# Kernel optimization log

Measured on AMD Instinct MI355X. Metric: run time of the kernel, lower is better.

## Reference

```python
import jax, jax.numpy as jnp
import numpy as np

CHANNEL = 16
KERNEL_SIZE = 5

def _gaussian3d_weight(channel, kernel_size):
    sigma = kernel_size / 6.0
    r = jnp.arange(-(kernel_size // 2), (kernel_size + 1) // 2, dtype=jnp.float32) ** 2
    # sum of squared offsets along each axis -> isotropic Gaussian
    k3 = r[None, None, :] + r[None, :, None] + r[:, None, None]
    k3 = jnp.exp(-k3 / (2.0 * sigma ** 2))
    k3 = k3 / k3.sum()
    # depthwise weight: [C_out=C, C_in/groups=1, kD, kH, kW]
    return jnp.broadcast_to(k3, (channel, 1, kernel_size, kernel_size, kernel_size))

def setup_inputs() -> dict:
    key = jax.random.key(0)
    x = jax.random.normal(key, (2, CHANNEL, 64, 128, 128), dtype=jnp.float32)
    weight = _gaussian3d_weight(CHANNEL, KERNEL_SIZE)
    return {"x": x, "weight": weight}

def reference(x, weight):
    # depthwise Conv3d, padding='same', groups=channel, no bias
    return jax.lax.conv_general_dilated(
        x, weight,
        window_strides=(1, 1, 1),
        padding='SAME',
        dimension_numbers=('NCDHW', 'OIDHW', 'NCDHW'),
        feature_group_count=CHANNEL,
    )
```

## Files before the change

kernel.cpp:

```cpp
#include <hip/hip_runtime.h>


#define DD 64
#define HH 128
#define WW 128
#define NC 16
#define ZCHUNK 16
#define SLICE (HH * WW)

typedef const __attribute__((address_space(1))) unsigned int g_u32;
typedef __attribute__((address_space(3))) unsigned int l_u32;

__global__ __launch_bounds__(256, 6)
void gauss3d_kernel(const float* __restrict__ x,
                    const float* __restrict__ wt,
                    float* __restrict__ out)
{
    __shared__ float raw[4][2][6][WW];
    __shared__ float wlds[16];

    const int tid  = threadIdx.x;
    const int w    = tid >> 6;
    const int lane = tid & 63;
    const int by   = blockIdx.x * 8;
    const int slab = blockIdx.y;
    const int z0   = blockIdx.z * ZCHUNK;
    const int ch   = slab & (NC - 1);

    const float* xs = x   + (size_t)slab * DD * SLICE;
    float*       os = out + (size_t)slab * DD * SLICE;

    if (tid < 15) {
        const int a = tid / 5, q = tid % 5;
        const float* wp = wt + ch * 125;
        float s = 0.f;
        for (int u = 0; u < 5; ++u)
            for (int v = 0; v < 5; ++v) {
                const int i0 = (a == 0) ? q : u;
                const int j0 = (a == 1) ? q : ((a == 0) ? u : v);
                const int k0 = (a == 2) ? q : v;
                s += wp[i0 * 25 + j0 * 5 + k0];
            }
        wlds[a * 5 + q] = s;
    }
    __syncthreads();

    const int sub    = lane >> 5;
    const int lane31 = lane & 31;
    const int col    = lane31 << 2;
    const int wy0    = by + w * 2;
    const int gy     = wy0 + sub;

    int so[3];
#pragma unroll
    for (int k = 0; k < 3; ++k) {
        const int gr = min(max(wy0 - 2 + 2 * k + sub, 0), HH - 1);
        so[k] = gr * WW + col;
    }

    float wzc[5], wxc[5], wyv[5];
#pragma unroll
    for (int i = 0; i < 5; ++i) {
        wzc[i] = wlds[i];
        wxc[i] = wlds[10 + i];
        const int r = gy - 2 + i;
        wyv[i] = (r >= 0 && r < HH) ? wlds[5 + i] : 0.f;
    }

    const int zbase = z0 - 2;

#define STAGE(ZS, B)                                                         \
    {                                                                        \
        const int zc = min(max((ZS), 0), DD - 1);                            \
        const float* sl = xs + (size_t)zc * SLICE;                           \
        _Pragma("unroll")                                                    \
        for (int k = 0; k < 3; ++k)                                          \
            __builtin_amdgcn_global_load_lds((g_u32*)(sl + so[k]),           \
                (l_u32*)(&raw[w][(B)][2 * k][0]), 16, 0, 0);                 \
    }

    float4 r0, r1, r2, r3, r4;
    r0 = r1 = r2 = r3 = r4 = make_float4(0.f, 0.f, 0.f, 0.f);

    STAGE(zbase, 0)

#define GSTEP(o0, o1, o2, o3, o4, I, WAIT)                                   \
    {                                                                        \
        const int zs = zbase + (I);                                          \
        STAGE(zs + 1, ((I) + 1) & 1)                                         \
        asm volatile("s_waitcnt vmcnt(" #WAIT ")" ::: "memory");             \
        __builtin_amdgcn_sched_barrier(0);                                   \
        float4 sv = make_float4(0.f, 0.f, 0.f, 0.f);                         \
        if ((unsigned)zs < (unsigned)DD) {               \
            const float (*rb)[WW] = raw[w][(I) & 1];                         \
            float4 yv = make_float4(0.f, 0.f, 0.f, 0.f);                     \
            _Pragma("unroll")                                                \
            for (int dy = 0; dy < 5; ++dy) {                                 \
                const float4 rv = *(const float4*)&rb[sub + dy][col];        \
                const float  wq = wyv[dy];                                   \
                yv.x += wq * rv.x; yv.y += wq * rv.y;                        \
                yv.z += wq * rv.z; yv.w += wq * rv.w;                        \
            }                                                                \
            float Lz = __shfl(yv.z, tid - 1, 64);                            \
            float Lw = __shfl(yv.w, tid - 1, 64);                            \
            float Rx = __shfl(yv.x, tid + 1, 64);                            \
            float Ry = __shfl(yv.y, tid + 1, 64);                            \
            if (lane31 == 0)  { Lz = 0.f; Lw = 0.f; }                        \
            if (lane31 == 31) { Rx = 0.f; Ry = 0.f; }                        \
            sv.x = wxc[0]*Lz   + wxc[1]*Lw   + wxc[2]*yv.x + wxc[3]*yv.y + wxc[4]*yv.z; \
            sv.y = wxc[0]*Lw   + wxc[1]*yv.x + wxc[2]*yv.y + wxc[3]*yv.z + wxc[4]*yv.w; \
            sv.z = wxc[0]*yv.x + wxc[1]*yv.y + wxc[2]*yv.z + wxc[3]*yv.w + wxc[4]*Rx;   \
            sv.w = wxc[0]*yv.y + wxc[1]*yv.z + wxc[2]*yv.w + wxc[3]*Rx   + wxc[4]*Ry;   \
        }                                                                    \
        o4 = sv;                                                             \
        const int zo = zs - 2;                                               \
        if (zo >= z0) {                                   \
            float4 ov;                                                       \
            ov.x = wzc[0]*o0.x + wzc[1]*o1.x + wzc[2]*o2.x + wzc[3]*o3.x + wzc[4]*o4.x; \
            ov.y = wzc[0]*o0.y + wzc[1]*o1.y + wzc[2]*o2.y + wzc[3]*o3.y + wzc[4]*o4.y; \
            ov.z = wzc[0]*o0.z + wzc[1]*o1.z + wzc[2]*o2.z + wzc[3]*o3.z + wzc[4]*o4.z; \
            ov.w = wzc[0]*o0.w + wzc[1]*o1.w + wzc[2]*o2.w + wzc[3]*o3.w + wzc[4]*o4.w; \
            *(float4*)(os + (size_t)zo * SLICE + (size_t)gy * WW + col) = ov;\
        }                                                                    \
        __builtin_amdgcn_s_barrier();    \
    }

    GSTEP(r1, r2, r3, r4, r0, 0, 3)
    GSTEP(r2, r3, r4, r0, r1, 1, 3)
    GSTEP(r3, r4, r0, r1, r2, 2, 3)
    GSTEP(r4, r0, r1, r2, r3, 3, 3)
    GSTEP(r0, r1, r2, r3, r4, 4, 3)
    GSTEP(r1, r2, r3, r4, r0, 5, 4)
    GSTEP(r2, r3, r4, r0, r1, 6, 4)
    GSTEP(r3, r4, r0, r1, r2, 7, 4)
    GSTEP(r4, r0, r1, r2, r3, 8, 4)
    GSTEP(r0, r1, r2, r3, r4, 9, 4)
    GSTEP(r1, r2, r3, r4, r0, 10, 4)
    GSTEP(r2, r3, r4, r0, r1, 11, 4)
    GSTEP(r3, r4, r0, r1, r2, 12, 4)
    GSTEP(r4, r0, r1, r2, r3, 13, 4)
    GSTEP(r0, r1, r2, r3, r4, 14, 4)
    GSTEP(r1, r2, r3, r4, r0, 15, 4)
    GSTEP(r2, r3, r4, r0, r1, 16, 4)
    GSTEP(r3, r4, r0, r1, r2, 17, 4)
    GSTEP(r4, r0, r1, r2, r3, 18, 4)
    GSTEP(r0, r1, r2, r3, r4, 19, 4)
#undef GSTEP
#undef STAGE
}

extern "C" void kernel_launch(void* const* d_in, const int* in_sizes, int n_in,
                              void* d_out, int out_size, void* d_ws, size_t ws_size,
                              hipStream_t stream)
{
    const float* x = (const float*)d_in[0];
    const float* w = (const float*)d_in[1];
    float*       o = (float*)d_out;

    dim3 grid(HH / 8, 2 * NC, DD / ZCHUNK);
    gauss3d_kernel<<<grid, 256, 0, stream>>>(x, w, o);
}
```

Measured before the change: 249.3 us.

## Compute four rows per wave and swizzle block order across slabs

Each wave now produces four output rows instead of two: it stages eight halo rows per z-slice and computes two row-pairs from them. This cuts redundant halo loads from 6 rows per 2 outputs to 8 per 4. The block size drops to 128 threads, and the flat block index is remapped so that consecutive blocks land on different slabs and z-chunks, which may spread memory traffic across channels. The cost is more registers (two sets of five z-history float4s) and fewer waves per block.

```diff
diff --git a/kernel.cpp b/kernel.cpp
--- a/kernel.cpp
+++ b/kernel.cpp
@@ -11,20 +11,23 @@
 typedef const __attribute__((address_space(1))) unsigned int g_u32;
 typedef __attribute__((address_space(3))) unsigned int l_u32;
 
-__global__ __launch_bounds__(256, 6)
+__global__ __launch_bounds__(128, 4)
 void gauss3d_kernel(const float* __restrict__ x,
                     const float* __restrict__ wt,
                     float* __restrict__ out)
 {
-    __shared__ float raw[4][2][6][WW];
+    __shared__ float raw[2][2][8][WW];
     __shared__ float wlds[16];
 
     const int tid  = threadIdx.x;
-    const int w    = tid >> 6;
+    const int wv   = tid >> 6;
     const int lane = tid & 63;
-    const int by   = blockIdx.x * 8;
-    const int slab = blockIdx.y;
-    const int z0   = blockIdx.z * ZCHUNK;
+
+    const int f  = blockIdx.x + (blockIdx.y << 4) + (blockIdx.z << 9);
+    const int g  = ((f & 7) << 8) + (f >> 3);
+    const int by   = (g & 15) * 8;
+    const int slab = (g >> 4) & 31;
+    const int z0   = (g >> 9) * ZCHUNK;
     const int ch   = slab & (NC - 1);
 
     const float* xs = x   + (size_t)slab * DD * SLICE;
@@ -48,23 +51,26 @@
     const int sub    = lane >> 5;
     const int lane31 = lane & 31;
     const int col    = lane31 << 2;
-    const int wy0    = by + w * 2;
-    const int gy     = wy0 + sub;
+    const int wy0    = by + wv * 4;
+    const int gyA    = wy0 + sub;
+    const int gyB    = wy0 + sub + 2;
 
-    int so[3];
+    int so[4];
 #pragma unroll
-    for (int k = 0; k < 3; ++k) {
+    for (int k = 0; k < 4; ++k) {
         const int gr = min(max(wy0 - 2 + 2 * k + sub, 0), HH - 1);
         so[k] = gr * WW + col;
     }
 
-    float wzc[5], wxc[5], wyv[5];
+    float wzc[5], wxc[5], wyvA[5], wyvB[5];
 #pragma unroll
     for (int i = 0; i < 5; ++i) {
         wzc[i] = wlds[i];
         wxc[i] = wlds[10 + i];
-        const int r = gy - 2 + i;
-        wyv[i] = (r >= 0 && r < HH) ? wlds[5 + i] : 0.f;
+        const int ra = gyA - 2 + i;
+        const int rb_ = gyB - 2 + i;
+        wyvA[i] = (ra  >= 0 && ra  < HH) ? wlds[5 + i] : 0.f;
+        wyvB[i] = (rb_ >= 0 && rb_ < HH) ? wlds[5 + i] : 0.f;
     }
 
     const int zbase = z0 - 2;
@@ -74,77 +80,97 @@
         const int zc = min(max((ZS), 0), DD - 1);                            \
         const float* sl = xs + (size_t)zc * SLICE;                           \
         _Pragma("unroll")                                                    \
-        for (int k = 0; k < 3; ++k)                                          \
+        for (int k = 0; k < 4; ++k)                                          \
             __builtin_amdgcn_global_load_lds((g_u32*)(sl + so[k]),           \
-                (l_u32*)(&raw[w][(B)][2 * k][0]), 16, 0, 0);                 \
+                (l_u32*)(&raw[wv][(B)][2 * k][0]), 16, 0, 0);                 \
     }
 
-    float4 r0, r1, r2, r3, r4;
-    r0 = r1 = r2 = r3 = r4 = make_float4(0.f, 0.f, 0.f, 0.f);
+    const float4 zero4 = make_float4(0.f, 0.f, 0.f, 0.f);
+
+    auto xp = [&](const float4& yv) -> float4 {
+        float Lz = __shfl(yv.z, lane - 1, 64);
+        float Lw = __shfl(yv.w, lane - 1, 64);
+        float Rx = __shfl(yv.x, lane + 1, 64);
+        float Ry = __shfl(yv.y, lane + 1, 64);
+        if (lane31 == 0)  { Lz = 0.f; Lw = 0.f; }
+        if (lane31 == 31) { Rx = 0.f; Ry = 0.f; }
+        float4 s;
+        s.x = wxc[0]*Lz   + wxc[1]*Lw   + wxc[2]*yv.x + wxc[3]*yv.y + wxc[4]*yv.z;
+        s.y = wxc[0]*Lw   + wxc[1]*yv.x + wxc[2]*yv.y + wxc[3]*yv.z + wxc[4]*yv.w;
+        s.z = wxc[0]*yv.x + wxc[1]*yv.y + wxc[2]*yv.z + wxc[3]*yv.w + wxc[4]*Rx;
+        s.w = wxc[0]*yv.y + wxc[1]*yv.z + wxc[2]*yv.w + wxc[3]*Rx   + wxc[4]*Ry;
+        return s;
+    };
+
+    float4 a0, a1, a2, a3, a4, b0, b1, b2, b3, b4;
+    a0 = a1 = a2 = a3 = a4 = zero4;
+    b0 = b1 = b2 = b3 = b4 = zero4;
 
     STAGE(zbase, 0)
 
-#define GSTEP(o0, o1, o2, o3, o4, I, WAIT)                                   \
+#define GSTEP(A0, A1, A2, A3, A4, B0, B1, B2, B3, B4, I, W)                  \
     {                                                                        \
         const int zs = zbase + (I);                                          \
         STAGE(zs + 1, ((I) + 1) & 1)                                         \
-        asm volatile("s_waitcnt vmcnt(" #WAIT ")" ::: "memory");             \
+        asm volatile("s_waitcnt vmcnt(" #W ")" ::: "memory");                \
         __builtin_amdgcn_sched_barrier(0);                                   \
-        float4 sv = make_float4(0.f, 0.f, 0.f, 0.f);                         \
+        float4 svA = zero4, svB = zero4;                                     \
         if ((unsigned)zs < (unsigned)DD) {               \
-            const float (*rb)[WW] = raw[w][(I) & 1];                         \
-            float4 yv = make_float4(0.f, 0.f, 0.f, 0.f);                     \
+            const float (*rb)[WW] = raw[wv][(I) & 1];                        \
+            float4 h[7];                                                     \
             _Pragma("unroll")                                                \
-            for (int dy = 0; dy < 5; ++dy) {                                 \
-                const float4 rv = *(const float4*)&rb[sub + dy][col];        \
-                const float  wq = wyv[dy];                                   \
-                yv.x += wq * rv.x; yv.y += wq * rv.y;                        \
-                yv.z += wq * rv.z; yv.w += wq * rv.w;                        \
+            for (int j = 0; j < 7; ++j)                                      \
+                h[j] = *(const float4*)&rb[sub + j][col];                    \
+            float4 yA = zero4, yB = zero4;                                   \
+            _Pragma("unroll")                                                \
+            for (int i = 0; i < 5; ++i) {                                    \
+                const float wa = wyvA[i], wb = wyvB[i];                      \
+                yA.x += wa * h[i].x;     yA.y += wa * h[i].y;                \
+                yA.z += wa * h[i].z;     yA.w += wa * h[i].w;                \
+                yB.x += wb * h[i + 2].x; yB.y += wb * h[i + 2].y;            \
+                yB.z += wb * h[i + 2].z; yB.w += wb * h[i + 2].w;            \
             }                                                                \
-            float Lz = __shfl(yv.z, tid - 1, 64);                            \
-            float Lw = __shfl(yv.w, tid - 1, 64);                            \
-            float Rx = __shfl(yv.x, tid + 1, 64);                            \
-            float Ry = __shfl(yv.y, tid + 1, 64);                            \
-            if (lane31 == 0)  { Lz = 0.f; Lw = 0.f; }                        \
-            if (lane31 == 31) { Rx = 0.f; Ry = 0.f; }                        \
-            sv.x = wxc[0]*Lz   + wxc[1]*Lw   + wxc[2]*yv.x + wxc[3]*yv.y + wxc[4]*yv.z; \
-            sv.y = wxc[0]*Lw   + wxc[1]*yv.x + wxc[2]*yv.y + wxc[3]*yv.z + wxc[4]*yv.w; \
-            sv.z = wxc[0]*yv.x + wxc[1]*yv.y + wxc[2]*yv.z + wxc[3]*yv.w + wxc[4]*Rx;   \
-            sv.w = wxc[0]*yv.y + wxc[1]*yv.z + wxc[2]*yv.w + wxc[3]*Rx   + wxc[4]*Ry;   \
+            svA = xp(yA);                                                    \
+            svB = xp(yB);                                                    \
         }                                                                    \
-        o4 = sv;                                                             \
+        A4 = svA; B4 = svB;                                                  \
         const int zo = zs - 2;                                               \
         if (zo >= z0) {                                   \
-            float4 ov;                                                       \
-            ov.x = wzc[0]*o0.x + wzc[1]*o1.x + wzc[2]*o2.x + wzc[3]*o3.x + wzc[4]*o4.x; \
-            ov.y = wzc[0]*o0.y + wzc[1]*o1.y + wzc[2]*o2.y + wzc[3]*o3.y + wzc[4]*o4.y; \
-            ov.z = wzc[0]*o0.z + wzc[1]*o1.z + wzc[2]*o2.z + wzc[3]*o3.z + wzc[4]*o4.z; \
-            ov.w = wzc[0]*o0.w + wzc[1]*o1.w + wzc[2]*o2.w + wzc[3]*o3.w + wzc[4]*o4.w; \
-            *(float4*)(os + (size_t)zo * SLICE + (size_t)gy * WW + col) = ov;\
+            float4 oA, oB;                                                   \
+            oA.x = wzc[0]*A0.x + wzc[1]*A1.x + wzc[2]*A2.x + wzc[3]*A3.x + wzc[4]*A4.x; \
+            oA.y = wzc[0]*A0.y + wzc[1]*A1.y + wzc[2]*A2.y + wzc[3]*A3.y + wzc[4]*A4.y; \
+            oA.z = wzc[0]*A0.z + wzc[1]*A1.z + wzc[2]*A2.z + wzc[3]*A3.z + wzc[4]*A4.z; \
+            oA.w = wzc[0]*A0.w + wzc[1]*A1.w + wzc[2]*A2.w + wzc[3]*A3.w + wzc[4]*A4.w; \
+            oB.x = wzc[0]*B0.x + wzc[1]*B1.x + wzc[2]*B2.x + wzc[3]*B3.x + wzc[4]*B4.x; \
+            oB.y = wzc[0]*B0.y + wzc[1]*B1.y + wzc[2]*B2.y + wzc[3]*B3.y + wzc[4]*B4.y; \
+            oB.z = wzc[0]*B0.z + wzc[1]*B1.z + wzc[2]*B2.z + wzc[3]*B3.z + wzc[4]*B4.z; \
+            oB.w = wzc[0]*B0.w + wzc[1]*B1.w + wzc[2]*B2.w + wzc[3]*B3.w + wzc[4]*B4.w; \
+            *(float4*)(os + (size_t)zo * SLICE + (size_t)gyA * WW + col) = oA; \
+            *(float4*)(os + (size_t)zo * SLICE + (size_t)gyB * WW + col) = oB; \
         }                                                                    \
         __builtin_amdgcn_s_barrier();    \
     }
 
-    GSTEP(r1, r2, r3, r4, r0, 0, 3)
-    GSTEP(r2, r3, r4, r0, r1, 1, 3)
-    GSTEP(r3, r4, r0, r1, r2, 2, 3)
-    GSTEP(r4, r0, r1, r2, r3, 3, 3)
-    GSTEP(r0, r1, r2, r3, r4, 4, 3)
-    GSTEP(r1, r2, r3, r4, r0, 5, 4)
-    GSTEP(r2, r3, r4, r0, r1, 6, 4)
-    GSTEP(r3, r4, r0, r1, r2, 7, 4)
-    GSTEP(r4, r0, r1, r2, r3, 8, 4)
-    GSTEP(r0, r1, r2, r3, r4, 9, 4)
-    GSTEP(r1, r2, r3, r4, r0, 10, 4)
-    GSTEP(r2, r3, r4, r0, r1, 11, 4)
-    GSTEP(r3, r4, r0, r1, r2, 12, 4)
-    GSTEP(r4, r0, r1, r2, r3, 13, 4)
-    GSTEP(r0, r1, r2, r3, r4, 14, 4)
-    GSTEP(r1, r2, r3, r4, r0, 15, 4)
-    GSTEP(r2, r3, r4, r0, r1, 16, 4)
-    GSTEP(r3, r4, r0, r1, r2, 17, 4)
-    GSTEP(r4, r0, r1, r2, r3, 18, 4)
-    GSTEP(r0, r1, r2, r3, r4, 19, 4)
+    GSTEP(a1, a2, a3, a4, a0, b1, b2, b3, b4, b0, 0, 4)
+    GSTEP(a2, a3, a4, a0, a1, b2, b3, b4, b0, b1, 1, 4)
+    GSTEP(a3, a4, a0, a1, a2, b3, b4, b0, b1, b2, 2, 4)
+    GSTEP(a4, a0, a1, a2, a3, b4, b0, b1, b2, b3, 3, 4)
+    GSTEP(a0, a1, a2, a3, a4, b0, b1, b2, b3, b4, 4, 4)
+    GSTEP(a1, a2, a3, a4, a0, b1, b2, b3, b4, b0, 5, 6)
+    GSTEP(a2, a3, a4, a0, a1, b2, b3, b4, b0, b1, 6, 6)
+    GSTEP(a3, a4, a0, a1, a2, b3, b4, b0, b1, b2, 7, 6)
+    GSTEP(a4, a0, a1, a2, a3, b4, b0, b1, b2, b3, 8, 6)
+    GSTEP(a0, a1, a2, a3, a4, b0, b1, b2, b3, b4, 9, 6)
+    GSTEP(a1, a2, a3, a4, a0, b1, b2, b3, b4, b0, 10, 6)
+    GSTEP(a2, a3, a4, a0, a1, b2, b3, b4, b0, b1, 11, 6)
+    GSTEP(a3, a4, a0, a1, a2, b3, b4, b0, b1, b2, 12, 6)
+    GSTEP(a4, a0, a1, a2, a3, b4, b0, b1, b2, b3, 13, 6)
+    GSTEP(a0, a1, a2, a3, a4, b0, b1, b2, b3, b4, 14, 6)
+    GSTEP(a1, a2, a3, a4, a0, b1, b2, b3, b4, b0, 15, 6)
+    GSTEP(a2, a3, a4, a0, a1, b2, b3, b4, b0, b1, 16, 6)
+    GSTEP(a3, a4, a0, a1, a2, b3, b4, b0, b1, b2, 17, 6)
+    GSTEP(a4, a0, a1, a2, a3, b4, b0, b1, b2, b3, 18, 6)
+    GSTEP(a0, a1, a2, a3, a4, b0, b1, b2, b3, b4, 19, 6)
 #undef GSTEP
 #undef STAGE
 }
@@ -158,5 +184,5 @@
     float*       o = (float*)d_out;
 
     dim3 grid(HH / 8, 2 * NC, DD / ZCHUNK);
-    gauss3d_kernel<<<grid, 256, 0, stream>>>(x, w, o);
+    gauss3d_kernel<<<grid, 128, 0, stream>>>(x, w, o);
 }
```

New measurement: 247.3 us. Within noise of the previous version (-0.8%).
